# Performance work log

Hardware: AMD Instinct MI355X
Metric: run time of the kernel (lower is better)

Reference implementation:

```python
import jax, jax.numpy as jnp
import numpy as np

# MANO prior contact vertex indices (f1+f2+f3+f4+f5+f0 from CMap_loss3)
_F1 = [697,698,699,700,712,713,714,715,737,738,739,740,741,743,744,745,746,748,749,750,753,754,755,756,757,758,759,760,761,762,763,764,765,766,767,768]
_F2 = [46,47,48,49,164,165,166,167,194,195,223,237,238,280,281,298,301,317,320,323,324,325,326,327,328,329,330,331,332,333,340,341,342,343,344,345,346,347,348,349,350,351,352,353,354,355]
_F3 = [356,357,358,359,375,376,386,387,396,397,402,403,413,429,433,434,435,436,437,438,439,440,441,442,443,444,452,453,454,455,456,459,460,461,462,463,464,465,466,467]
_F4 = [468,469,470,471,484,485,486,496,497,506,507,513,514,524,545,546,547,548,549,550,551,552,553,555,563,564,565,566,567,570,572,573,574,575,576,577,578]
_F5 = [580,581,582,583,600,601,602,614,615,624,625,630,631,641,663,664,665,666,667,668,670,672,680,681,682,683,684,686,687,688,689,690,691,692,693,694,695]
_F0 = [73,96,98,99,772,774,775,777]
PRIOR_IDX = np.array(_F1 + _F2 + _F3 + _F4 + _F5 + _F0, dtype=np.int32)


def _sqdist(a, b):
    # a: [B,N,3], b: [B,M,3] -> squared distances [B,N,M] via ||a||^2+||b||^2-2ab
    a2 = jnp.sum(a * a, -1)          # [B,N]
    b2 = jnp.sum(b * b, -1)          # [B,M]
    ab = jnp.einsum('bnd,bmd->bnm', a, b)
    return jnp.maximum(a2[:, :, None] + b2[:, None, :] - 2.0 * ab, 0.0)


def _knn1(src, trg):
    # nearest neighbor (K=1): squared dists + indices, like pytorch3d knn_points
    d2 = _sqdist(src, trg)           # [B,N,M]
    return jnp.min(d2, -1), jnp.argmin(d2, -1)


def _verts_normals(verts, faces):
    # area-weighted vertex normals (pytorch3d verts_normals_packed)
    v0 = verts[:, faces[:, 0]]       # [B,F,3]
    v1 = verts[:, faces[:, 1]]
    v2 = verts[:, faces[:, 2]]
    fn = jnp.cross(v1 - v0, v2 - v0)
    vn = jnp.zeros_like(verts)
    vn = vn.at[:, faces[:, 0]].add(fn).at[:, faces[:, 1]].add(fn).at[:, faces[:, 2]].add(fn)
    return vn / (jnp.linalg.norm(vn, axis=-1, keepdims=True) + 1e-12)


def setup_inputs() -> dict:
    key = jax.random.key(0)
    ks = jax.random.split(key, 8)
    B, N1, V, F, Z, P = 64, 8192, 778, 1538, 64, 61
    scale = 0.1  # keep points in a 0.1 box so contact thresholds (0.005/0.01) fire
    return {
        'obj_xyz': jax.random.uniform(ks[0], (B, N1, 3), jnp.float32) * scale,
        'recon_xyz': jax.random.uniform(ks[1], (B, V, 3), jnp.float32) * scale,
        'gt_xyz': jax.random.uniform(ks[2], (B, V, 3), jnp.float32) * scale,
        'mean': jax.random.normal(ks[3], (B, Z), jnp.float32),
        'log_var': jax.random.normal(ks[4], (B, Z), jnp.float32),
        'recon_param': jax.random.normal(ks[5], (B, P), jnp.float32),
        'x_param': jax.random.normal(ks[6], (B, P), jnp.float32),
        'faces': jax.random.randint(ks[7], (F, 3), 0, V, jnp.int32),
    }


def reference(obj_xyz, recon_xyz, gt_xyz, mean, log_var, recon_param, x_param, faces):
    B = obj_xyz.shape[0]
    fB = jnp.float32(B)

    # KNN from object points to gt / reconstructed hand (squared dists)
    d_gt, _ = _knn1(obj_xyz, gt_xyz)            # [B,N1]
    d_rec, idx_rec = _knn1(obj_xyz, recon_xyz)  # [B,N1], [B,N1]

    # param loss: MSE sum / B
    param_loss = jnp.sum((recon_param - x_param) ** 2) / fB

    # CVAE loss: chamfer (point_reduction='sum', batch_reduction='mean') + KLD
    d2 = _sqdist(recon_xyz, gt_xyz)             # [B,778,778]
    recon_loss = jnp.mean(jnp.sum(jnp.min(d2, -1), -1)) + jnp.mean(jnp.sum(jnp.min(d2, -2), -1))
    KLD = -0.5 * jnp.sum(1.0 + log_var - mean ** 2 - jnp.exp(log_var)) / fB * 10.0
    cvae_loss = recon_loss + KLD

    # CMap_loss3: obj NN distance to prior hand contact verts, masked by cmap
    cmap = d_rec < 0.01 ** 2                    # [B,N1] bool
    prior = recon_xyz[:, PRIOR_IDX, :]          # [B,222,3]
    obj_CD, _ = _knn1(obj_xyz, prior)           # [B,N1]
    n_points = jnp.sum(cmap).astype(jnp.float32)
    cmap_loss = 3000.0 * jnp.sum(jnp.where(cmap, obj_CD, 0.0)) / (fB * n_points)

    # CMap consistency: contact-map overlap ratio
    recon_cmap = jnp.sqrt(d_rec) < 0.005
    gt_cmap = jnp.sqrt(d_gt) < 0.005
    gt_cnum = jnp.sum(gt_cmap).astype(jnp.float32) + 0.0001
    consistency_loss = -5.0 * jnp.sum(recon_cmap & gt_cmap).astype(jnp.float32) / gt_cnum

    # inter-penetration: gather NN hand verts/normals, sign of dot, masked dist sum
    vn = _verts_normals(recon_xyz, faces)                               # [B,778,3]
    nn_v = jnp.take_along_axis(recon_xyz, idx_rec[..., None], axis=1)   # [B,N1,3]
    nn_n = jnp.take_along_axis(vn, idx_rec[..., None], axis=1)          # [B,N1,3]
    interior = jnp.sum((nn_v - obj_xyz) * nn_n, -1) > 0                 # [B,N1]
    penetr_loss = 100.0 * jnp.sum(jnp.where(interior, d_rec, 0.0)) / fB

    a, b, c, d, e = 1.0, 0.1, 1000.0, 10.0, 10.0
    loss = a * cvae_loss + b * param_loss + c * cmap_loss + d * consistency_loss + e * penetr_loss
    return loss
```

## Files before the change

### kernel.cpp

```cpp
#include <hip/hip_runtime.h>
#include <math.h>

#define NB     64
#define N1V    8192
#define NPTS   (NB * N1V)
#define NV     778
#define NVP    780
#define NQ     195
#define SEG1Q  51
#define NFACE  1538
#define NZ     64
#define NPAR   61
#define NPRIOR 204
#define PPT    8
#define BIAS   0.0625f

#define REC_BLOCKS 256
#define GT_BLOCKS  256
#define CH_BLOCKS  128
#define NROLE_BLOCKS (REC_BLOCKS + GT_BLOCKS + CH_BLOCKS)
#define CMB_BLOCKS 64

#define BATCH_F4 2352
#define ACC_OFF (NB * BATCH_F4 * 4)
#define RC_OFF  (ACC_OFF + 16)
#define GC_OFF  (RC_OFF + NPTS / 32)

__device__ __constant__ int c_prior[NPRIOR] = {
  697,698,699,700,712,713,714,715,737,738,739,740,741,743,744,745,746,748,749,750,
  753,754,755,756,757,758,759,760,761,762,763,764,765,766,767,768,
  46,47,48,49,164,165,166,167,194,195,223,237,238,280,281,298,301,317,320,323,
  324,325,326,327,328,329,330,331,332,333,340,341,342,343,344,345,346,347,348,349,
  350,351,352,353,354,355,
  356,357,358,359,375,376,386,387,396,397,402,403,413,429,433,434,435,436,437,438,
  439,440,441,442,443,444,452,453,454,455,456,459,460,461,462,463,464,465,466,467,
  468,469,470,471,484,485,486,496,497,506,507,513,514,524,545,546,547,548,549,550,
  551,552,553,555,563,564,565,566,567,570,572,573,574,575,576,577,578,
  580,581,582,583,600,601,602,614,615,624,625,630,631,641,663,664,665,666,667,668,
  670,672,680,681,682,683,684,686,687,688,689,690,691,692,693,694,695,
  73,96,98,99,772,774,775,777
};

__global__ __launch_bounds__(256) void k_prep(const float* __restrict__ recon,
                                              const float* __restrict__ gt,
                                              const int* __restrict__ faces,
                                              float4* __restrict__ ws4,
                                              float* __restrict__ acc) {
    int b = blockIdx.x, tid = threadIdx.x;
    if (b == 0 && tid < 16) acc[tid] = 0.0f;
    __shared__ float4 s_r[NV];
    __shared__ float s_vnx[NV], s_vny[NV], s_vnz[NV];
    __shared__ unsigned int s_bm[25];
    __shared__ unsigned short s_pre[26];
    __shared__ unsigned short s_perm[NV];

    if (tid < 25) s_bm[tid] = 0u;
    __syncthreads();
    if (tid < NPRIOR) {
        int v = c_prior[tid];
        atomicOr(&s_bm[v >> 5], 1u << (v & 31));
    }
    const float* rb = recon + (size_t)b * NV * 3;
    const float* gb = gt    + (size_t)b * NV * 3;
    float4* gt4   = ws4 + (size_t)b * BATCH_F4;
    float4* rec4p = gt4 + NVP;
    float4* nrm4p = rec4p + NVP;
    for (int j = tid; j < NV; j += 256) {
        float x = rb[3*j], y = rb[3*j+1], z = rb[3*j+2];
        s_r[j] = make_float4(x, y, z, x*x + y*y + z*z + BIAS);
        x = gb[3*j]; y = gb[3*j+1]; z = gb[3*j+2];
        gt4[j] = make_float4(x, y, z, x*x + y*y + z*z);
        s_vnx[j] = 0.0f; s_vny[j] = 0.0f; s_vnz[j] = 0.0f;
    }
    if (tid < 2) gt4[NV + tid] = make_float4(0.f, 0.f, 0.f, 1e30f);
    __syncthreads();
    if (tid == 0) {
        unsigned int run = 0;
        for (int w = 0; w < 25; ++w) { s_pre[w] = (unsigned short)run; run += __popc(s_bm[w]); }
        s_pre[25] = (unsigned short)run;
    }
    __syncthreads();
    for (int j = tid; j < NV; j += 256) {
        int w = j >> 5;
        unsigned int below = s_bm[w] & ((1u << (j & 31)) - 1u);
        int rank = s_pre[w] + __popc(below);
        bool member = (s_bm[w] >> (j & 31)) & 1u;
        int pos = member ? rank : (NPRIOR + (j - rank));
        s_perm[pos] = (unsigned short)j;
    }
    for (int f = tid; f < NFACE; f += 256) {
        int i0 = faces[3*f], i1 = faces[3*f+1], i2 = faces[3*f+2];
        float4 p0 = s_r[i0], p1 = s_r[i1], p2 = s_r[i2];
        float e1x = p1.x - p0.x, e1y = p1.y - p0.y, e1z = p1.z - p0.z;
        float e2x = p2.x - p0.x, e2y = p2.y - p0.y, e2z = p2.z - p0.z;
        float fx = e1y * e2z - e1z * e2y;
        float fy = e1z * e2x - e1x * e2z;
        float fz = e1x * e2y - e1y * e2x;
        atomicAdd(&s_vnx[i0], fx); atomicAdd(&s_vny[i0], fy); atomicAdd(&s_vnz[i0], fz);
        atomicAdd(&s_vnx[i1], fx); atomicAdd(&s_vny[i1], fy); atomicAdd(&s_vnz[i1], fz);
        atomicAdd(&s_vnx[i2], fx); atomicAdd(&s_vny[i2], fy); atomicAdd(&s_vnz[i2], fz);
    }
    __syncthreads();
    for (int j = tid; j < NVP; j += 256) {
        if (j < NV) {
            int src = s_perm[j];
            rec4p[j] = s_r[src];
            float x = s_vnx[src], y = s_vny[src], z = s_vnz[src];
            float inv = 1.0f / (sqrtf(x*x + y*y + z*z) + 1e-12f);
            nrm4p[j] = make_float4(x * inv, y * inv, z * inv, 0.0f);
        } else {
            rec4p[j] = make_float4(0.f, 0.f, 0.f, 1e30f);
            nrm4p[j] = make_float4(0.f, 0.f, 1.f, 0.0f);
        }
    }
}

#define LOAD_PTS(ob)                                                          \
    const float4* ob4 = (const float4*)((ob) + (size_t)tid * 24);             \
    float4 q0 = ob4[0], q1 = ob4[1], q2 = ob4[2],                             \
           q3 = ob4[3], q4 = ob4[4], q5 = ob4[5];                             \
    float px[PPT], py[PPT], pz[PPT];                                          \
    px[0]=q0.x; py[0]=q0.y; pz[0]=q0.z;  px[1]=q0.w; py[1]=q1.x; pz[1]=q1.y;  \
    px[2]=q1.z; py[2]=q1.w; pz[2]=q2.x;  px[3]=q2.y; py[3]=q2.z; pz[3]=q2.w;  \
    px[4]=q3.x; py[4]=q3.y; pz[4]=q3.z;  px[5]=q3.w; py[5]=q4.x; pz[5]=q4.y;  \
    px[6]=q4.z; py[6]=q4.w; pz[6]=q5.x;  px[7]=q5.y; py[7]=q5.z; pz[7]=q5.w;

__global__ __launch_bounds__(256) void k_fused(const float* __restrict__ obj,
                                               const float4* __restrict__ ws4,
                                               float* __restrict__ acc,
                                               unsigned char* __restrict__ rcA,
                                               unsigned char* __restrict__ gcA) {
    __shared__ float4 s_t[NVP];
    __shared__ float s_red[3];
    int tid = threadIdx.x;
    int blk = blockIdx.x;

    if (blk < REC_BLOCKS) {
        int b = blk >> 2, chunk = blk & 3;
        const float4* base = ws4 + (size_t)b * BATCH_F4;
        const float4* rec4p = base + NVP;
        const float4* nrm4p = base + 2 * NVP;
        for (int j = tid; j < NVP; j += 256) s_t[j] = rec4p[j];
        if (tid < 3) s_red[tid] = 0.0f;
        __syncthreads();

        const float* ob = obj + ((size_t)b * N1V + (size_t)chunk * 2048) * 3;
        LOAD_PTS(ob)
        float nax[PPT], nay[PPT], naz[PPT], m[PPT];
        int q[PPT];
#pragma unroll
        for (int i = 0; i < PPT; ++i) {
            nax[i] = -2.0f * px[i]; nay[i] = -2.0f * py[i]; naz[i] = -2.0f * pz[i];
            m[i] = 3.4e38f; q[i] = 0;
        }
        float mp[PPT];
#pragma unroll 1
        for (int jq = 0; jq < SEG1Q; ++jq) {
            int j = 4 * jq;
            float4 t0 = s_t[j], t1 = s_t[j+1], t2 = s_t[j+2], t3 = s_t[j+3];
#pragma unroll
            for (int i = 0; i < PPT; ++i) {
                float d0 = fmaf(nax[i], t0.x, fmaf(nay[i], t0.y, fmaf(naz[i], t0.z, t0.w)));
                float d1 = fmaf(nax[i], t1.x, fmaf(nay[i], t1.y, fmaf(naz[i], t1.z, t1.w)));
                float d2 = fmaf(nax[i], t2.x, fmaf(nay[i], t2.y, fmaf(naz[i], t2.z, t2.w)));
                float d3 = fmaf(nax[i], t3.x, fmaf(nay[i], t3.y, fmaf(naz[i], t3.z, t3.w)));
                float mn = fminf(fminf(fminf(d0, d1), fminf(d2, d3)), m[i]);
                q[i] = (mn < m[i]) ? jq : q[i];
                m[i] = mn;
            }
        }
#pragma unroll
        for (int i = 0; i < PPT; ++i) mp[i] = m[i];
#pragma unroll 1
        for (int jq = SEG1Q; jq < NQ; ++jq) {
            int j = 4 * jq;
            float4 t0 = s_t[j], t1 = s_t[j+1], t2 = s_t[j+2], t3 = s_t[j+3];
#pragma unroll
            for (int i = 0; i < PPT; ++i) {
                float d0 = fmaf(nax[i], t0.x, fmaf(nay[i], t0.y, fmaf(naz[i], t0.z, t0.w)));
                float d1 = fmaf(nax[i], t1.x, fmaf(nay[i], t1.y, fmaf(naz[i], t1.z, t1.w)));
                float d2 = fmaf(nax[i], t2.x, fmaf(nay[i], t2.y, fmaf(naz[i], t2.z, t2.w)));
                float d3 = fmaf(nax[i], t3.x, fmaf(nay[i], t3.y, fmaf(naz[i], t3.z, t3.w)));
                float mn = fminf(fminf(fminf(d0, d1), fminf(d2, d3)), m[i]);
                q[i] = (mn < m[i]) ? jq : q[i];
                m[i] = mn;
            }
        }
        float lS_cmap = 0.0f, lN_cmap = 0.0f, lS_pen = 0.0f;
        unsigned int rcbits = 0;
#pragma unroll
        for (int i = 0; i < PPT; ++i) {
            float a2 = px[i]*px[i] + py[i]*py[i] + pz[i]*pz[i];
            float drec = fmaxf(a2 + (m[i]  - BIAS), 0.0f);
            float dpri = fmaxf(a2 + (mp[i] - BIAS), 0.0f);
            bool cm = drec < 1e-4f;
            bool rc = sqrtf(drec) < 0.005f;
            if (cm) { lS_cmap += dpri; lN_cmap += 1.0f; }
            if (rc) rcbits |= (1u << i);
            int jr = 4 * q[i];
            float4 t0 = s_t[jr], t1 = s_t[jr+1], t2 = s_t[jr+2], t3 = s_t[jr+3];
            float d0 = fmaf(nax[i], t0.x, fmaf(nay[i], t0.y, fmaf(naz[i], t0.z, t0.w)));
            float d1 = fmaf(nax[i], t1.x, fmaf(nay[i], t1.y, fmaf(naz[i], t1.z, t1.w)));
            float d2 = fmaf(nax[i], t2.x, fmaf(nay[i], t2.y, fmaf(naz[i], t2.z, t2.w)));
            float d3 = fmaf(nax[i], t3.x, fmaf(nay[i], t3.y, fmaf(naz[i], t3.z, t3.w)));
            float mmin = fminf(fminf(d0, d1), fminf(d2, d3));
            int off = (d0 == mmin) ? 0 : ((d1 == mmin) ? 1 : ((d2 == mmin) ? 2 : 3));
            int jstar = jr + off;
            float4 tS = s_t[jstar];
            float4 nr = nrm4p[jstar];
            float ddot = (tS.x - px[i]) * nr.x + (tS.y - py[i]) * nr.y
                       + (tS.z - pz[i]) * nr.z;
            if (ddot > 0.0f) lS_pen += drec;
        }
        rcA[(size_t)blk * 256 + tid] = (unsigned char)rcbits;
        atomicAdd(&s_red[0], lS_cmap);
        atomicAdd(&s_red[1], lN_cmap);
        atomicAdd(&s_red[2], lS_pen);
        __syncthreads();
        if (tid == 0) atomicAdd(&acc[3], s_red[0]);
        if (tid == 1) atomicAdd(&acc[4], s_red[1]);
        if (tid == 2) atomicAdd(&acc[7], s_red[2]);
        return;
    }

    if (blk < REC_BLOCKS + GT_BLOCKS) {
        int r = blk - REC_BLOCKS;
        int b = r >> 2, chunk = r & 3;
        const float4* gt4v = ws4 + (size_t)b * BATCH_F4;
        for (int j = tid; j < NVP; j += 256) s_t[j] = gt4v[j];
        if (tid == 0) s_red[0] = 0.0f;
        __syncthreads();

        const float* ob = obj + ((size_t)b * N1V + (size_t)chunk * 2048) * 3;
        LOAD_PTS(ob)
        float nax[PPT], nay[PPT], naz[PPT], mgt[PPT];
#pragma unroll
        for (int i = 0; i < PPT; ++i) {
            nax[i] = -2.0f * px[i]; nay[i] = -2.0f * py[i]; naz[i] = -2.0f * pz[i];
            mgt[i] = 3.4e38f;
        }
#pragma unroll 1
        for (int jq = 0; jq < NQ; ++jq) {
            int j = 4 * jq;
            float4 t0 = s_t[j], t1 = s_t[j+1], t2 = s_t[j+2], t3 = s_t[j+3];
#pragma unroll
            for (int i = 0; i < PPT; ++i) {
                float d0 = fmaf(nax[i], t0.x, fmaf(nay[i], t0.y, fmaf(naz[i], t0.z, t0.w)));
                float d1 = fmaf(nax[i], t1.x, fmaf(nay[i], t1.y, fmaf(naz[i], t1.z, t1.w)));
                float d2 = fmaf(nax[i], t2.x, fmaf(nay[i], t2.y, fmaf(naz[i], t2.z, t2.w)));
                float d3 = fmaf(nax[i], t3.x, fmaf(nay[i], t3.y, fmaf(naz[i], t3.z, t3.w)));
                mgt[i] = fminf(fminf(mgt[i], fminf(d0, d1)), fminf(d2, d3));
            }
        }
        float lN_gt = 0.0f;
        unsigned int gcbits = 0;
#pragma unroll
        for (int i = 0; i < PPT; ++i) {
            float a2 = px[i]*px[i] + py[i]*py[i] + pz[i]*pz[i];
            float dgt = fmaxf(a2 + mgt[i], 0.0f);
            if (sqrtf(dgt) < 0.005f) { lN_gt += 1.0f; gcbits |= (1u << i); }
        }
        gcA[(size_t)r * 256 + tid] = (unsigned char)gcbits;
        atomicAdd(&s_red[0], lN_gt);
        __syncthreads();
        if (tid == 0) atomicAdd(&acc[5], s_red[0]);
        return;
    }

    {
        int c   = blk - (REC_BLOCKS + GT_BLOCKS);
        int b   = c >> 1;
        int dir = c & 1;
        const float4* base = ws4 + (size_t)b * BATCH_F4;
        const float4* srcv = dir ? base : (base + NVP);
        const float4* tgtv = dir ? (base + NVP) : base;
        for (int j = tid; j < NVP; j += 256) s_t[j] = tgtv[j];
        if (tid == 0) s_red[0] = 0.0f;
        __syncthreads();

        const int CPT = 4;
        float nax[CPT], nay[CPT], naz[CPT], a2[CPT], m[CPT];
        bool valid[CPT];
#pragma unroll
        for (int k = 0; k < CPT; ++k) {
            int p = tid + 256 * k;
            valid[k] = (p < NV);
            float4 s = srcv[valid[k] ? p : 0];
            nax[k] = -2.0f * s.x; nay[k] = -2.0f * s.y; naz[k] = -2.0f * s.z;
            a2[k] = s.w;
            m[k] = 3.4e38f;
        }
#pragma unroll 1
        for (int j = 0; j < NVP; j += 4) {
            float4 t0 = s_t[j], t1 = s_t[j+1], t2 = s_t[j+2], t3 = s_t[j+3];
#pragma unroll
            for (int k = 0; k < CPT; ++k) {
                float d0 = fmaf(nax[k], t0.x, fmaf(nay[k], t0.y, fmaf(naz[k], t0.z, t0.w)));
                float d1 = fmaf(nax[k], t1.x, fmaf(nay[k], t1.y, fmaf(naz[k], t1.z, t1.w)));
                float d2 = fmaf(nax[k], t2.x, fmaf(nay[k], t2.y, fmaf(naz[k], t2.z, t2.w)));
                float d3 = fmaf(nax[k], t3.x, fmaf(nay[k], t3.y, fmaf(naz[k], t3.z, t3.w)));
                m[k] = fminf(fminf(m[k], fminf(d0, d1)), fminf(d2, d3));
            }
        }
        float local = 0.0f;
#pragma unroll
        for (int k = 0; k < CPT; ++k)
            if (valid[k]) local += fmaxf(a2[k] + m[k] - BIAS, 0.0f);
        atomicAdd(&s_red[0], local);
        __syncthreads();
        if (tid == 0) atomicAdd(&acc[2], s_red[0]);
    }
}

__global__ __launch_bounds__(256) void k_combine(float* __restrict__ acc,
                                                 const unsigned int* __restrict__ rcW,
                                                 const unsigned int* __restrict__ gcW,
                                                 const float* __restrict__ mean,
                                                 const float* __restrict__ log_var,
                                                 const float* __restrict__ rp,
                                                 const float* __restrict__ xp,
                                                 float* __restrict__ out) {
    int blk = blockIdx.x, tid = threadIdx.x;
    __shared__ float s_red[2];
    __shared__ unsigned int s_ticket;
    if (tid < 2) s_red[tid] = 0.0f;
    __syncthreads();
    int idx = blk * 256 + tid;
    unsigned int rc = rcW[idx], gc = gcW[idx];
    float cnt = (float)__popc(rc & gc);
    atomicAdd(&s_red[0], cnt);
    __syncthreads();
    if (tid == 0) atomicAdd(&acc[6], s_red[0]);
    __threadfence();
    if (tid == 0) s_ticket = atomicAdd((unsigned int*)&acc[15], 1u);
    __syncthreads();

    if (s_ticket == CMB_BLOCKS - 1) {
        if (tid < 2) s_red[tid] = 0.0f;
        __syncthreads();
        float s_param = 0.0f, s_kld = 0.0f;
        for (int i = tid; i < NB * NPAR; i += 256) {
            float d = rp[i] - xp[i];
            s_param += d * d;
        }
        for (int i = tid; i < NB * NZ; i += 256) {
            float m = mean[i], lv = log_var[i];
            s_kld += 1.0f + lv - m * m - expf(lv);
        }
        atomicAdd(&s_red[0], s_param);
        atomicAdd(&s_red[1], s_kld);
        __syncthreads();
        if (tid == 0) {
            const float fB = 64.0f;
            float a2v = atomicAdd(&acc[2], 0.0f);
            float a3  = atomicAdd(&acc[3], 0.0f);
            float a4  = atomicAdd(&acc[4], 0.0f);
            float a5  = atomicAdd(&acc[5], 0.0f);
            float a6  = atomicAdd(&acc[6], 0.0f);
            float a7  = atomicAdd(&acc[7], 0.0f);
            float param_loss  = s_red[0] / fB;
            float KLD         = -0.5f * s_red[1] / fB * 10.0f;
            float recon_loss  = a2v / fB;
            float cmap_loss   = 3000.0f * a3 / (fB * a4);
            float consistency = -5.0f * a6 / (a5 + 0.0001f);
            float penetr      = 100.0f * a7 / fB;
            out[0] = (recon_loss + KLD) + 0.1f * param_loss + 1000.0f * cmap_loss
                   + 10.0f * consistency + 10.0f * penetr;
        }
    }
}

extern "C" void kernel_launch(void* const* d_in, const int* in_sizes, int n_in,
                              void* d_out, int out_size, void* d_ws, size_t ws_size,
                              hipStream_t stream) {
    (void)in_sizes; (void)n_in; (void)out_size; (void)ws_size;
    const float* obj     = (const float*)d_in[0];
    const float* recon   = (const float*)d_in[1];
    const float* gt      = (const float*)d_in[2];
    const float* mean    = (const float*)d_in[3];
    const float* log_var = (const float*)d_in[4];
    const float* rp      = (const float*)d_in[5];
    const float* xp      = (const float*)d_in[6];
    const int*   faces   = (const int*)d_in[7];
    float4* ws4 = (float4*)d_ws;
    float* acc  = (float*)d_ws + ACC_OFF;
    unsigned char* rcA = (unsigned char*)((float*)d_ws + RC_OFF);
    unsigned char* gcA = (unsigned char*)((float*)d_ws + GC_OFF);
    float* out  = (float*)d_out;

    k_prep   <<<NB,           256, 0, stream>>>(recon, gt, faces, ws4, acc);
    k_fused  <<<NROLE_BLOCKS, 256, 0, stream>>>(obj, ws4, acc, rcA, gcA);
    k_combine<<<CMB_BLOCKS,   256, 0, stream>>>(acc, (const unsigned int*)rcA,
                                                (const unsigned int*)gcA,
                                                mean, log_var, rp, xp, out);
}
```

Baseline: 197.4 us.

## Replace brute-force nearest-neighbor search with per-batch uniform grid spatial lookup

```diff
diff --git a/kernel.cpp b/kernel.cpp
--- a/kernel.cpp
+++ b/kernel.cpp
@@ -6,25 +6,27 @@
 #define NPTS   (NB * N1V)
 #define NV     778
 #define NVP    780
-#define NQ     195
-#define SEG1Q  51
 #define NFACE  1538
 #define NZ     64
 #define NPAR   61
 #define NPRIOR 204
-#define PPT    8
+#define PPT    4
+#define GRES   8
+#define GH     0.0125f
+#define GINV   80.0f
+#define SLACK  1e-6f
 #define BIAS   0.0625f
 
-#define REC_BLOCKS 256
-#define GT_BLOCKS  256
+#define REC_BLOCKS 512
+#define GT_BLOCKS  512
 #define CH_BLOCKS  128
-#define NROLE_BLOCKS (REC_BLOCKS + GT_BLOCKS + CH_BLOCKS)
+#define NROLE (REC_BLOCKS + GT_BLOCKS + CH_BLOCKS)
 #define CMB_BLOCKS 64
 
-#define BATCH_F4 2352
+#define BATCH_F4 2688
 #define ACC_OFF (NB * BATCH_F4 * 4)
 #define RC_OFF  (ACC_OFF + 16)
-#define GC_OFF  (RC_OFF + NPTS / 32)
+#define GC_OFF  (RC_OFF + 32768)
 
 __device__ __constant__ int c_prior[NPRIOR] = {
   697,698,699,700,712,713,714,715,737,738,739,740,741,743,744,745,746,748,749,750,
@@ -41,6 +43,62 @@
   73,96,98,99,772,774,775,777
 };
 
+__device__ __forceinline__ int cell_of(float x, float y, float z) {
+    int cx = (int)(x * GINV); cx = min(GRES - 1, max(0, cx));
+    int cy = (int)(y * GINV); cy = min(GRES - 1, max(0, cy));
+    int cz = (int)(z * GINV); cz = min(GRES - 1, max(0, cz));
+    return (cz * GRES + cy) * GRES + cx;
+}
+
+template<bool WIDX>
+__device__ __forceinline__ float grid_min(float px, float py, float pz,
+                                          float nax, float nay, float naz, float a2,
+                                          const float4* __restrict__ sp,
+                                          const unsigned short* __restrict__ cs,
+                                          int* bi_out) {
+    int cx = (int)(px * GINV); cx = min(7, max(0, cx));
+    int cy = (int)(py * GINV); cy = min(7, max(0, cy));
+    int cz = (int)(pz * GINV); cz = min(7, max(0, cz));
+    float best = 3.4e38f; int bi = 0;
+#pragma unroll 1
+    for (int r = 1; r <= 2; ++r) {
+        int x0 = max(0, cx - r), x1 = min(7, cx + r);
+        int y0 = max(0, cy - r), y1 = min(7, cy + r);
+        int z0 = max(0, cz - r), z1 = min(7, cz + r);
+#pragma unroll 1
+        for (int z = z0; z <= z1; ++z)
+#pragma unroll 1
+        for (int y = y0; y <= y1; ++y) {
+            int base = (z * 8 + y) * 8;
+            int s = cs[base + x0], e = cs[base + x1 + 1];
+#pragma unroll 1
+            for (int t = s; t < e; ++t) {
+                float4 q = sp[t];
+                float d = fmaf(nax, q.x, fmaf(nay, q.y, fmaf(naz, q.z, q.w)));
+                if (WIDX) { if (d < best) { best = d; bi = t; } }
+                else best = fminf(best, d);
+            }
+        }
+        float b0 = (cx - r >= 0) ? (px - (float)(cx - r) * GH) : 1e30f;
+        float b1 = (cx + r <= 7) ? ((float)(cx + r + 1) * GH - px) : 1e30f;
+        float b2 = (cy - r >= 0) ? (py - (float)(cy - r) * GH) : 1e30f;
+        float b3 = (cy + r <= 7) ? ((float)(cy + r + 1) * GH - py) : 1e30f;
+        float b4 = (cz - r >= 0) ? (pz - (float)(cz - r) * GH) : 1e30f;
+        float b5 = (cz + r <= 7) ? ((float)(cz + r + 1) * GH - pz) : 1e30f;
+        float bm = fminf(fminf(fminf(b0, b1), fminf(b2, b3)), fminf(b4, b5));
+        if (a2 + best + SLACK < bm * bm) { if (WIDX) *bi_out = bi; return best; }
+    }
+#pragma unroll 1
+    for (int t = 0; t < NV; ++t) {
+        float4 q = sp[t];
+        float d = fmaf(nax, q.x, fmaf(nay, q.y, fmaf(naz, q.z, q.w)));
+        if (WIDX) { if (d < best) { best = d; bi = t; } }
+        else best = fminf(best, d);
+    }
+    if (WIDX) *bi_out = bi;
+    return best;
+}
+
 __global__ __launch_bounds__(256) void k_prep(const float* __restrict__ recon,
                                               const float* __restrict__ gt,
                                               const int* __restrict__ faces,
@@ -50,44 +108,28 @@
     if (b == 0 && tid < 16) acc[tid] = 0.0f;
     __shared__ float4 s_r[NV];
     __shared__ float s_vnx[NV], s_vny[NV], s_vnz[NV];
-    __shared__ unsigned int s_bm[25];
-    __shared__ unsigned short s_pre[26];
-    __shared__ unsigned short s_perm[NV];
-
-    if (tid < 25) s_bm[tid] = 0u;
-    __syncthreads();
-    if (tid < NPRIOR) {
-        int v = c_prior[tid];
-        atomicOr(&s_bm[v >> 5], 1u << (v & 31));
-    }
+    __shared__ unsigned int s_cnt[512];
+    __shared__ unsigned short s_start[513];
+
+    float4* base4 = ws4 + (size_t)b * BATCH_F4;
+    float4* recS = base4;
+    float4* nrmS = base4 + NVP;
+    float4* gtS  = base4 + 2 * NVP;
+    float4* priS = base4 + 3 * NVP;
+    unsigned short* rcs = (unsigned short*)(base4 + 2544 / 4 * 4 + 0);
+    rcs = (unsigned short*)(ws4 + (size_t)b * BATCH_F4 + 2544);
+    unsigned short* gcs = rcs + 520;
+
     const float* rb = recon + (size_t)b * NV * 3;
     const float* gb = gt    + (size_t)b * NV * 3;
-    float4* gt4   = ws4 + (size_t)b * BATCH_F4;
-    float4* rec4p = gt4 + NVP;
-    float4* nrm4p = rec4p + NVP;
+
     for (int j = tid; j < NV; j += 256) {
         float x = rb[3*j], y = rb[3*j+1], z = rb[3*j+2];
-        s_r[j] = make_float4(x, y, z, x*x + y*y + z*z + BIAS);
-        x = gb[3*j]; y = gb[3*j+1]; z = gb[3*j+2];
-        gt4[j] = make_float4(x, y, z, x*x + y*y + z*z);
+        s_r[j] = make_float4(x, y, z, x*x + y*y + z*z);
         s_vnx[j] = 0.0f; s_vny[j] = 0.0f; s_vnz[j] = 0.0f;
     }
-    if (tid < 2) gt4[NV + tid] = make_float4(0.f, 0.f, 0.f, 1e30f);
-    __syncthreads();
-    if (tid == 0) {
-        unsigned int run = 0;
-        for (int w = 0; w < 25; ++w) { s_pre[w] = (unsigned short)run; run += __popc(s_bm[w]); }
-        s_pre[25] = (unsigned short)run;
-    }
-    __syncthreads();
-    for (int j = tid; j < NV; j += 256) {
-        int w = j >> 5;
-        unsigned int below = s_bm[w] & ((1u << (j & 31)) - 1u);
-        int rank = s_pre[w] + __popc(below);
-        bool member = (s_bm[w] >> (j & 31)) & 1u;
-        int pos = member ? rank : (NPRIOR + (j - rank));
-        s_perm[pos] = (unsigned short)j;
-    }
+    s_cnt[tid] = 0u; s_cnt[tid + 256] = 0u;
+    __syncthreads();
     for (int f = tid; f < NFACE; f += 256) {
         int i0 = faces[3*f], i1 = faces[3*f+1], i2 = faces[3*f+2];
         float4 p0 = s_r[i0], p1 = s_r[i1], p2 = s_r[i2];
@@ -101,113 +143,142 @@
         atomicAdd(&s_vnx[i2], fx); atomicAdd(&s_vny[i2], fy); atomicAdd(&s_vnz[i2], fz);
     }
     __syncthreads();
-    for (int j = tid; j < NVP; j += 256) {
-        if (j < NV) {
-            int src = s_perm[j];
-            rec4p[j] = s_r[src];
-            float x = s_vnx[src], y = s_vny[src], z = s_vnz[src];
-            float inv = 1.0f / (sqrtf(x*x + y*y + z*z) + 1e-12f);
-            nrm4p[j] = make_float4(x * inv, y * inv, z * inv, 0.0f);
-        } else {
-            rec4p[j] = make_float4(0.f, 0.f, 0.f, 1e30f);
-            nrm4p[j] = make_float4(0.f, 0.f, 1.f, 0.0f);
-        }
-    }
-}
-
-#define LOAD_PTS(ob)                                                          \
-    const float4* ob4 = (const float4*)((ob) + (size_t)tid * 24);             \
-    float4 q0 = ob4[0], q1 = ob4[1], q2 = ob4[2],                             \
-           q3 = ob4[3], q4 = ob4[4], q5 = ob4[5];                             \
+    for (int j = tid; j < NV; j += 256) {
+        float x = s_vnx[j], y = s_vny[j], z = s_vnz[j];
+        float inv = 1.0f / (sqrtf(x*x + y*y + z*z) + 1e-12f);
+        s_vnx[j] = x * inv; s_vny[j] = y * inv; s_vnz[j] = z * inv;
+    }
+    for (int j = tid; j < NV; j += 256) {
+        float4 v = s_r[j];
+        atomicAdd(&s_cnt[cell_of(v.x, v.y, v.z)], 1u);
+    }
+    __syncthreads();
+    for (int off = 1; off < 512; off <<= 1) {
+        unsigned int a0 = (tid >= off) ? s_cnt[tid - off] : 0u;
+        int i2 = tid + 256;
+        unsigned int a1 = (i2 >= off) ? s_cnt[i2 - off] : 0u;
+        __syncthreads();
+        s_cnt[tid] += a0; s_cnt[i2] += a1;
+        __syncthreads();
+    }
+    if (tid == 0) s_start[0] = 0;
+    s_start[tid + 1]   = (unsigned short)s_cnt[tid];
+    s_start[tid + 257] = (unsigned short)s_cnt[tid + 256];
+    __syncthreads();
+    rcs[tid] = s_start[tid]; rcs[tid + 256] = s_start[tid + 256];
+    if (tid == 0) rcs[512] = s_start[512];
+    s_cnt[tid] = 0u; s_cnt[tid + 256] = 0u;
+    __syncthreads();
+    for (int j = tid; j < NV; j += 256) {
+        float4 v = s_r[j];
+        int c = cell_of(v.x, v.y, v.z);
+        int pos = (int)s_start[c] + (int)atomicAdd(&s_cnt[c], 1u);
+        recS[pos] = v;
+        nrmS[pos] = make_float4(s_vnx[j], s_vny[j], s_vnz[j], 0.0f);
+    }
+    for (int k = tid; k < NPRIOR; k += 256) priS[k] = s_r[c_prior[k]];
+    __syncthreads();
+
+    for (int j = tid; j < NV; j += 256) {
+        float x = gb[3*j], y = gb[3*j+1], z = gb[3*j+2];
+        s_r[j] = make_float4(x, y, z, x*x + y*y + z*z);
+    }
+    s_cnt[tid] = 0u; s_cnt[tid + 256] = 0u;
+    __syncthreads();
+    for (int j = tid; j < NV; j += 256) {
+        float4 v = s_r[j];
+        atomicAdd(&s_cnt[cell_of(v.x, v.y, v.z)], 1u);
+    }
+    __syncthreads();
+    for (int off = 1; off < 512; off <<= 1) {
+        unsigned int a0 = (tid >= off) ? s_cnt[tid - off] : 0u;
+        int i2 = tid + 256;
+        unsigned int a1 = (i2 >= off) ? s_cnt[i2 - off] : 0u;
+        __syncthreads();
+        s_cnt[tid] += a0; s_cnt[i2] += a1;
+        __syncthreads();
+    }
+    if (tid == 0) s_start[0] = 0;
+    s_start[tid + 1]   = (unsigned short)s_cnt[tid];
+    s_start[tid + 257] = (unsigned short)s_cnt[tid + 256];
+    __syncthreads();
+    gcs[tid] = s_start[tid]; gcs[tid + 256] = s_start[tid + 256];
+    if (tid == 0) gcs[512] = s_start[512];
+    s_cnt[tid] = 0u; s_cnt[tid + 256] = 0u;
+    __syncthreads();
+    for (int j = tid; j < NV; j += 256) {
+        float4 v = s_r[j];
+        int c = cell_of(v.x, v.y, v.z);
+        int pos = (int)s_start[c] + (int)atomicAdd(&s_cnt[c], 1u);
+        gtS[pos] = v;
+    }
+}
+
+#define LOAD_PTS4(ob)                                                         \
+    const float4* ob4 = (const float4*)((ob) + (size_t)tid * 12);             \
+    float4 q0 = ob4[0], q1 = ob4[1], q2 = ob4[2];                             \
     float px[PPT], py[PPT], pz[PPT];                                          \
     px[0]=q0.x; py[0]=q0.y; pz[0]=q0.z;  px[1]=q0.w; py[1]=q1.x; pz[1]=q1.y;  \
-    px[2]=q1.z; py[2]=q1.w; pz[2]=q2.x;  px[3]=q2.y; py[3]=q2.z; pz[3]=q2.w;  \
-    px[4]=q3.x; py[4]=q3.y; pz[4]=q3.z;  px[5]=q3.w; py[5]=q4.x; pz[5]=q4.y;  \
-    px[6]=q4.z; py[6]=q4.w; pz[6]=q5.x;  px[7]=q5.y; py[7]=q5.z; pz[7]=q5.w;
+    px[2]=q1.z; py[2]=q1.w; pz[2]=q2.x;  px[3]=q2.y; py[3]=q2.z; pz[3]=q2.w;
 
 __global__ __launch_bounds__(256) void k_fused(const float* __restrict__ obj,
                                                const float4* __restrict__ ws4,
                                                float* __restrict__ acc,
                                                unsigned char* __restrict__ rcA,
                                                unsigned char* __restrict__ gcA) {
-    __shared__ float4 s_t[NVP];
+    __shared__ float4 s_pts[NVP];
+    __shared__ float4 s_pri[NPRIOR];
+    __shared__ unsigned short s_cs[514];
     __shared__ float s_red[3];
     int tid = threadIdx.x;
     int blk = blockIdx.x;
 
     if (blk < REC_BLOCKS) {
-        int b = blk >> 2, chunk = blk & 3;
-        const float4* base = ws4 + (size_t)b * BATCH_F4;
-        const float4* rec4p = base + NVP;
-        const float4* nrm4p = base + 2 * NVP;
-        for (int j = tid; j < NVP; j += 256) s_t[j] = rec4p[j];
+        int b = blk >> 3, chunk = blk & 7;
+        const float4* base4 = ws4 + (size_t)b * BATCH_F4;
+        const unsigned short* rcs = (const unsigned short*)(ws4 + (size_t)b * BATCH_F4 + 2544);
+        for (int j = tid; j < NV; j += 256) s_pts[j] = base4[j];
+        for (int k = tid; k < NPRIOR; k += 256) s_pri[k] = base4[3 * NVP + k];
         if (tid < 3) s_red[tid] = 0.0f;
-        __syncthreads();
-
-        const float* ob = obj + ((size_t)b * N1V + (size_t)chunk * 2048) * 3;
-        LOAD_PTS(ob)
-        float nax[PPT], nay[PPT], naz[PPT], m[PPT];
-        int q[PPT];
+        for (int t = tid; t < 513; t += 256) s_cs[t] = rcs[t];
+        __syncthreads();
+
+        const float* ob = obj + ((size_t)b * N1V + (size_t)chunk * 1024) * 3;
+        LOAD_PTS4(ob)
+        float nax[PPT], nay[PPT], naz[PPT], a2[PPT], mpri[PPT];
 #pragma unroll
         for (int i = 0; i < PPT; ++i) {
             nax[i] = -2.0f * px[i]; nay[i] = -2.0f * py[i]; naz[i] = -2.0f * pz[i];
-            m[i] = 3.4e38f; q[i] = 0;
-        }
-        float mp[PPT];
-#pragma unroll 1
-        for (int jq = 0; jq < SEG1Q; ++jq) {
+            a2[i] = px[i]*px[i] + py[i]*py[i] + pz[i]*pz[i];
+            mpri[i] = 3.4e38f;
+        }
+#pragma unroll 1
+        for (int jq = 0; jq < NPRIOR / 4; ++jq) {
             int j = 4 * jq;
-            float4 t0 = s_t[j], t1 = s_t[j+1], t2 = s_t[j+2], t3 = s_t[j+3];
+            float4 t0 = s_pri[j], t1 = s_pri[j+1], t2 = s_pri[j+2], t3 = s_pri[j+3];
 #pragma unroll
             for (int i = 0; i < PPT; ++i) {
                 float d0 = fmaf(nax[i], t0.x, fmaf(nay[i], t0.y, fmaf(naz[i], t0.z, t0.w)));
                 float d1 = fmaf(nax[i], t1.x, fmaf(nay[i], t1.y, fmaf(naz[i], t1.z, t1.w)));
                 float d2 = fmaf(nax[i], t2.x, fmaf(nay[i], t2.y, fmaf(naz[i], t2.z, t2.w)));
                 float d3 = fmaf(nax[i], t3.x, fmaf(nay[i], t3.y, fmaf(naz[i], t3.z, t3.w)));
-                float mn = fminf(fminf(fminf(d0, d1), fminf(d2, d3)), m[i]);
-                q[i] = (mn < m[i]) ? jq : q[i];
-                m[i] = mn;
-            }
-        }
-#pragma unroll
-        for (int i = 0; i < PPT; ++i) mp[i] = m[i];
-#pragma unroll 1
-        for (int jq = SEG1Q; jq < NQ; ++jq) {
-            int j = 4 * jq;
-            float4 t0 = s_t[j], t1 = s_t[j+1], t2 = s_t[j+2], t3 = s_t[j+3];
-#pragma unroll
-            for (int i = 0; i < PPT; ++i) {
-                float d0 = fmaf(nax[i], t0.x, fmaf(nay[i], t0.y, fmaf(naz[i], t0.z, t0.w)));
-                float d1 = fmaf(nax[i], t1.x, fmaf(nay[i], t1.y, fmaf(naz[i], t1.z, t1.w)));
-                float d2 = fmaf(nax[i], t2.x, fmaf(nay[i], t2.y, fmaf(naz[i], t2.z, t2.w)));
-                float d3 = fmaf(nax[i], t3.x, fmaf(nay[i], t3.y, fmaf(naz[i], t3.z, t3.w)));
-                float mn = fminf(fminf(fminf(d0, d1), fminf(d2, d3)), m[i]);
-                q[i] = (mn < m[i]) ? jq : q[i];
-                m[i] = mn;
+                mpri[i] = fminf(fminf(mpri[i], fminf(d0, d1)), fminf(d2, d3));
             }
         }
         float lS_cmap = 0.0f, lN_cmap = 0.0f, lS_pen = 0.0f;
         unsigned int rcbits = 0;
-#pragma unroll
+        const float4* nrmG = base4 + NVP;
+#pragma unroll 1
         for (int i = 0; i < PPT; ++i) {
-            float a2 = px[i]*px[i] + py[i]*py[i] + pz[i]*pz[i];
-            float drec = fmaxf(a2 + (m[i]  - BIAS), 0.0f);
-            float dpri = fmaxf(a2 + (mp[i] - BIAS), 0.0f);
-            bool cm = drec < 1e-4f;
-            bool rc = sqrtf(drec) < 0.005f;
-            if (cm) { lS_cmap += dpri; lN_cmap += 1.0f; }
-            if (rc) rcbits |= (1u << i);
-            int jr = 4 * q[i];
-            float4 t0 = s_t[jr], t1 = s_t[jr+1], t2 = s_t[jr+2], t3 = s_t[jr+3];
-            float d0 = fmaf(nax[i], t0.x, fmaf(nay[i], t0.y, fmaf(naz[i], t0.z, t0.w)));
-            float d1 = fmaf(nax[i], t1.x, fmaf(nay[i], t1.y, fmaf(naz[i], t1.z, t1.w)));
-            float d2 = fmaf(nax[i], t2.x, fmaf(nay[i], t2.y, fmaf(naz[i], t2.z, t2.w)));
-            float d3 = fmaf(nax[i], t3.x, fmaf(nay[i], t3.y, fmaf(naz[i], t3.z, t3.w)));
-            float mmin = fminf(fminf(d0, d1), fminf(d2, d3));
-            int off = (d0 == mmin) ? 0 : ((d1 == mmin) ? 1 : ((d2 == mmin) ? 2 : 3));
-            int jstar = jr + off;
-            float4 tS = s_t[jstar];
-            float4 nr = nrm4p[jstar];
+            int bi;
+            float bp = grid_min<true>(px[i], py[i], pz[i], nax[i], nay[i], naz[i],
+                                      a2[i], s_pts, s_cs, &bi);
+            float drec = fmaxf(a2[i] + bp, 0.0f);
+            float dpri = fmaxf(a2[i] + mpri[i], 0.0f);
+            if (drec < 1e-4f) { lS_cmap += dpri; lN_cmap += 1.0f; }
+            if (sqrtf(drec) < 0.005f) rcbits |= (1u << i);
+            float4 tS = s_pts[bi];
+            float4 nr = nrmG[bi];
             float ddot = (tS.x - px[i]) * nr.x + (tS.y - py[i]) * nr.y
                        + (tS.z - pz[i]) * nr.z;
             if (ddot > 0.0f) lS_pen += drec;
@@ -225,39 +296,25 @@
 
     if (blk < REC_BLOCKS + GT_BLOCKS) {
         int r = blk - REC_BLOCKS;
-        int b = r >> 2, chunk = r & 3;
-        const float4* gt4v = ws4 + (size_t)b * BATCH_F4;
-        for (int j = tid; j < NVP; j += 256) s_t[j] = gt4v[j];
+        int b = r >> 3, chunk = r & 7;
+        const float4* base4 = ws4 + (size_t)b * BATCH_F4;
+        const unsigned short* gcs = (const unsigned short*)(ws4 + (size_t)b * BATCH_F4 + 2544) + 520;
+        for (int j = tid; j < NV; j += 256) s_pts[j] = base4[2 * NVP + j];
+        for (int t = tid; t < 513; t += 256) s_cs[t] = gcs[t];
         if (tid == 0) s_red[0] = 0.0f;
         __syncthreads();
 
-        const float* ob = obj + ((size_t)b * N1V + (size_t)chunk * 2048) * 3;
-        LOAD_PTS(ob)
-        float nax[PPT], nay[PPT], naz[PPT], mgt[PPT];
-#pragma unroll
-        for (int i = 0; i < PPT; ++i) {
-            nax[i] = -2.0f * px[i]; nay[i] = -2.0f * py[i]; naz[i] = -2.0f * pz[i];
-            mgt[i] = 3.4e38f;
-        }
-#pragma unroll 1
-        for (int jq = 0; jq < NQ; ++jq) {
-            int j = 4 * jq;
-            float4 t0 = s_t[j], t1 = s_t[j+1], t2 = s_t[j+2], t3 = s_t[j+3];
-#pragma unroll
-            for (int i = 0; i < PPT; ++i) {
-                float d0 = fmaf(nax[i], t0.x, fmaf(nay[i], t0.y, fmaf(naz[i], t0.z, t0.w)));
-                float d1 = fmaf(nax[i], t1.x, fmaf(nay[i], t1.y, fmaf(naz[i], t1.z, t1.w)));
-                float d2 = fmaf(nax[i], t2.x, fmaf(nay[i], t2.y, fmaf(naz[i], t2.z, t2.w)));
-                float d3 = fmaf(nax[i], t3.x, fmaf(nay[i], t3.y, fmaf(naz[i], t3.z, t3.w)));
-                mgt[i] = fminf(fminf(mgt[i], fminf(d0, d1)), fminf(d2, d3));
-            }
-        }
+        const float* ob = obj + ((size_t)b * N1V + (size_t)chunk * 1024) * 3;
+        LOAD_PTS4(ob)
         float lN_gt = 0.0f;
         unsigned int gcbits = 0;
-#pragma unroll
+#pragma unroll 1
         for (int i = 0; i < PPT; ++i) {
+            float nax = -2.0f * px[i], nay = -2.0f * py[i], naz = -2.0f * pz[i];
             float a2 = px[i]*px[i] + py[i]*py[i] + pz[i]*pz[i];
-            float dgt = fmaxf(a2 + mgt[i], 0.0f);
+            float bp = grid_min<false>(px[i], py[i], pz[i], nax, nay, naz,
+                                       a2, s_pts, s_cs, (int*)0);
+            float dgt = fmaxf(a2 + bp, 0.0f);
             if (sqrtf(dgt) < 0.005f) { lN_gt += 1.0f; gcbits |= (1u << i); }
         }
         gcA[(size_t)r * 256 + tid] = (unsigned char)gcbits;
@@ -271,15 +328,17 @@
         int c   = blk - (REC_BLOCKS + GT_BLOCKS);
         int b   = c >> 1;
         int dir = c & 1;
-        const float4* base = ws4 + (size_t)b * BATCH_F4;
-        const float4* srcv = dir ? base : (base + NVP);
-        const float4* tgtv = dir ? (base + NVP) : base;
-        for (int j = tid; j < NVP; j += 256) s_t[j] = tgtv[j];
+        extern const float* __unused_dummy;
+        const float4* base4 = ws4 + (size_t)b * BATCH_F4;
+        const float4* srcv = dir ? (base4 + 2 * NVP) : base4;
+        const float4* tgtv = dir ? base4 : (base4 + 2 * NVP);
+        for (int j = tid; j < NV; j += 256) s_pts[j] = tgtv[j];
+        if (tid < 2) s_pts[NV + tid] = make_float4(0.f, 0.f, 0.f, 1e30f);
         if (tid == 0) s_red[0] = 0.0f;
         __syncthreads();
 
         const int CPT = 4;
-        float nax[CPT], nay[CPT], naz[CPT], a2[CPT], m[CPT];
+        float nax[CPT], nay[CPT], naz[CPT], a2s[CPT], m[CPT];
         bool valid[CPT];
 #pragma unroll
         for (int k = 0; k < CPT; ++k) {
@@ -287,12 +346,12 @@
             valid[k] = (p < NV);
             float4 s = srcv[valid[k] ? p : 0];
             nax[k] = -2.0f * s.x; nay[k] = -2.0f * s.y; naz[k] = -2.0f * s.z;
-            a2[k] = s.w;
+            a2s[k] = s.x*s.x + s.y*s.y + s.z*s.z;
             m[k] = 3.4e38f;
         }
 #pragma unroll 1
         for (int j = 0; j < NVP; j += 4) {
-            float4 t0 = s_t[j], t1 = s_t[j+1], t2 = s_t[j+2], t3 = s_t[j+3];
+            float4 t0 = s_pts[j], t1 = s_pts[j+1], t2 = s_pts[j+2], t3 = s_pts[j+3];
 #pragma unroll
             for (int k = 0; k < CPT; ++k) {
                 float d0 = fmaf(nax[k], t0.x, fmaf(nay[k], t0.y, fmaf(naz[k], t0.z, t0.w)));
@@ -305,7 +364,7 @@
         float local = 0.0f;
 #pragma unroll
         for (int k = 0; k < CPT; ++k)
-            if (valid[k]) local += fmaxf(a2[k] + m[k] - BIAS, 0.0f);
+            if (valid[k]) local += fmaxf(a2s[k] + m[k], 0.0f);
         atomicAdd(&s_red[0], local);
         __syncthreads();
         if (tid == 0) atomicAdd(&acc[2], s_red[0]);
@@ -325,9 +384,9 @@
     __shared__ unsigned int s_ticket;
     if (tid < 2) s_red[tid] = 0.0f;
     __syncthreads();
-    int idx = blk * 256 + tid;
-    unsigned int rc = rcW[idx], gc = gcW[idx];
-    float cnt = (float)__popc(rc & gc);
+    float cnt = 0.0f;
+    for (int i = blk * 256 + tid; i < 32768; i += CMB_BLOCKS * 256)
+        cnt += (float)__popc(rcW[i] & gcW[i]);
     atomicAdd(&s_red[0], cnt);
     __syncthreads();
     if (tid == 0) atomicAdd(&acc[6], s_red[0]);
@@ -388,9 +447,9 @@
     unsigned char* gcA = (unsigned char*)((float*)d_ws + GC_OFF);
     float* out  = (float*)d_out;
 
-    k_prep   <<<NB,           256, 0, stream>>>(recon, gt, faces, ws4, acc);
-    k_fused  <<<NROLE_BLOCKS, 256, 0, stream>>>(obj, ws4, acc, rcA, gcA);
-    k_combine<<<CMB_BLOCKS,   256, 0, stream>>>(acc, (const unsigned int*)rcA,
-                                                (const unsigned int*)gcA,
-                                                mean, log_var, rp, xp, out);
-}
+    k_prep   <<<NB,         256, 0, stream>>>(recon, gt, faces, ws4, acc);
+    k_fused  <<<NROLE,      256, 0, stream>>>(obj, ws4, acc, rcA, gcA);
+    k_combine<<<CMB_BLOCKS, 256, 0, stream>>>(acc, (const unsigned int*)rcA,
+                                              (const unsigned int*)gcA,
+                                              mean, log_var, rp, xp, out);
+}
```

After: 206.6 us. +4.7%, slower.
